# Optimization experiments

Measured on AMD Instinct MI355X. Metric: run time of the kernel, lower is better.

Reference implementation:

```python
import jax, jax.numpy as jnp
import numpy as np

N = 100000   # nodes
E = 1600000  # directed edges (before self loops)
IN = 64
HID = 32     # per-head hidden channels
H = 4        # heads
OUT = 32     # final output channels
NEG_SLOPE = 0.2
LN_EPS = 1e-5


def setup_inputs() -> dict:
    key = jax.random.key(0)
    ks = jax.random.split(key, 24)
    def nrm(k, shape, s=0.1):
        return jax.random.normal(k, shape, jnp.float32) * s
    inp = {
        "x": jax.random.normal(ks[0], (N, IN), jnp.float32),
        "edge_index": jax.random.randint(ks[1], (2, E), 0, N, jnp.int32),
    }
    in_dims = [IN, H * HID, H * HID]
    j = 2
    for i, di in enumerate(in_dims):
        inp[f"W{i}"] = nrm(ks[j], (di, H * HID)); j += 1
        inp[f"as{i}"] = nrm(ks[j], (H, HID)); j += 1
        inp[f"ad{i}"] = nrm(ks[j], (H, HID)); j += 1
        inp[f"b{i}"] = jnp.zeros((H * HID,), jnp.float32)
        inp[f"g{i}"] = jnp.ones((H * HID,), jnp.float32)
        inp[f"be{i}"] = jnp.zeros((H * HID,), jnp.float32)
    inp["Wf"] = nrm(ks[j], (H * HID, OUT)); j += 1
    inp["asf"] = nrm(ks[j], (1, OUT)); j += 1
    inp["adf"] = nrm(ks[j], (1, OUT)); j += 1
    inp["bf"] = jnp.zeros((OUT,), jnp.float32)
    return inp


def gat_conv(x, src, dst, W, att_s, att_d, bias, heads, C, concat, n_nodes):
    # h: [N, H, C]
    h = (x @ W).reshape(n_nodes, heads, C)
    a_src = jnp.sum(h * att_s, axis=-1)  # [N, H]
    a_dst = jnp.sum(h * att_d, axis=-1)  # [N, H]
    e = jax.nn.leaky_relu(a_src[src] + a_dst[dst], NEG_SLOPE)  # [E', H]
    # segment softmax over incoming edges of each dst node
    m = jax.ops.segment_max(e, dst, num_segments=n_nodes)
    m = jnp.where(jnp.isfinite(m), m, 0.0)
    ex = jnp.exp(e - m[dst])
    denom = jax.ops.segment_sum(ex, dst, num_segments=n_nodes)
    alpha = ex / (denom[dst] + 1e-16)  # [E', H]
    msg = h[src] * alpha[..., None]    # [E', H, C]
    out = jax.ops.segment_sum(msg, dst, num_segments=n_nodes)  # [N, H, C]
    if concat:
        out = out.reshape(n_nodes, heads * C)
    else:
        out = out.mean(axis=1)
    return out + bias


def layer_norm(x, g, b):
    mu = x.mean(-1, keepdims=True)
    v = jnp.mean((x - mu) ** 2, axis=-1, keepdims=True)
    return g * (x - mu) / jnp.sqrt(v + LN_EPS) + b


def reference(x, edge_index,
              W0, as0, ad0, b0, g0, be0,
              W1, as1, ad1, b1, g1, be1,
              W2, as2, ad2, b2, g2, be2,
              Wf, asf, adf, bf):
    n_nodes = x.shape[0]
    loop = jnp.arange(n_nodes, dtype=edge_index.dtype)
    src = jnp.concatenate([edge_index[0], loop])  # add self loops (PyG default)
    dst = jnp.concatenate([edge_index[1], loop])
    blocks = [(W0, as0, ad0, b0, g0, be0),
              (W1, as1, ad1, b1, g1, be1),
              (W2, as2, ad2, b2, g2, be2)]
    for (W, a_s, a_d, b, g, be) in blocks:
        x = gat_conv(x, src, dst, W, a_s, a_d, b, H, HID, True, n_nodes)
        x = jax.nn.elu(layer_norm(x, g, be))
    return gat_conv(x, src, dst, Wf, asf, adf, bf, 1, OUT, False, n_nodes)
```

## Files before the change

### kernel.cpp

```cpp
#include <hip/hip_runtime.h>
#include <hip/hip_bf16.h>

constexpr int NN   = 100000;
constexpr int EE   = 1600000;
constexpr int ETOT = EE + NN;
constexpr float SLOPE = 0.2f;
constexpr int BSH = 10;
constexpr int NB  = (NN + (1 << BSH) - 1) >> BSH;
constexpr int CCH = 8192;

typedef __attribute__((ext_vector_type(8))) short short8;
typedef __attribute__((ext_vector_type(4))) float f32x4;

__device__ __forceinline__ float bf_lo(unsigned u) { return __uint_as_float(u << 16); }
__device__ __forceinline__ float bf_hi(unsigned u) { return __uint_as_float(u & 0xffff0000u); }
__device__ __forceinline__ unsigned short f2bf(float f) {
    __hip_bfloat16 h = __float2bfloat16(f);
    return *(unsigned short*)&h;
}
__device__ __forceinline__ void wave_lds_fence() {
    __asm__ volatile("s_waitcnt lgkmcnt(0)" ::: "memory");
}

__global__ void k_cvt_x(const float* __restrict__ x, unsigned short* __restrict__ xb) {
    int i = blockIdx.x * blockDim.x + threadIdx.x;
    if (i >= NN * 64 / 8) return;
    const float4* xp = (const float4*)(x + (size_t)i * 8);
    float4 v0 = xp[0], v1 = xp[1];
    unsigned short o[8] = {f2bf(v0.x), f2bf(v0.y), f2bf(v0.z), f2bf(v0.w),
                           f2bf(v1.x), f2bf(v1.y), f2bf(v1.z), f2bf(v1.w)};
    *(uint4*)(xb + (size_t)i * 8) = *(uint4*)o;
}

__global__ void k_cvt_wt(const float* __restrict__ W, unsigned short* __restrict__ Wt,
                         int K, int N) {
    int i = blockIdx.x * blockDim.x + threadIdx.x;
    if (i >= K * N) return;
    int k = i / N, n = i % N;
    Wt[(size_t)n * K + k] = f2bf(W[i]);
}

__global__ void k_zero(int* p, int n) {
    int i = blockIdx.x * blockDim.x + threadIdx.x;
    if (i < n) p[i] = 0;
}

__global__ __launch_bounds__(256) void k_bhist(const int* __restrict__ ei,
                                               int* __restrict__ gbh) {
    __shared__ int h[NB];
    int t = threadIdx.x;
    if (t < NB) h[t] = 0;
    __syncthreads();
    int i = blockIdx.x * 2048 + t;
#pragma unroll
    for (int k = 0; k < 8; k++, i += 256)
        if (i < EE) atomicAdd(&h[ei[EE + i] >> BSH], 1);
    __syncthreads();
    if (t < NB && h[t]) atomicAdd(&gbh[t], h[t]);
}

__global__ void k_bscan(const int* __restrict__ gbh, int* __restrict__ ebase,
                        int* __restrict__ gcur) {
    __shared__ int sd[128];
    int t = threadIdx.x;
    int v = (t < NB) ? gbh[t] : 0;
    sd[t] = v;
    __syncthreads();
    for (int off = 1; off < 128; off <<= 1) {
        int x = (t >= off) ? sd[t - off] : 0;
        __syncthreads();
        sd[t] += x;
        __syncthreads();
    }
    int ex = sd[t] - v;
    if (t < NB) { ebase[t] = ex; gcur[t] = ex; }
    if (t == NB) ebase[NB] = EE;
}

__global__ __launch_bounds__(256) void k_bscatter(const int* __restrict__ ei,
                                                  int* __restrict__ gcur,
                                                  int* __restrict__ pbuf) {
    __shared__ int h[NB], base[NB], cur[NB];
    int t = threadIdx.x;
    if (t < NB) { h[t] = 0; cur[t] = 0; }
    __syncthreads();
    int c0 = blockIdx.x * CCH;
    int cend = c0 + CCH < EE ? c0 + CCH : EE;
    for (int i = c0 + t; i < cend; i += 256)
        atomicAdd(&h[ei[EE + i] >> BSH], 1);
    __syncthreads();
    if (t < NB && h[t] > 0) base[t] = atomicAdd(&gcur[t], h[t]);
    __syncthreads();
    for (int i = c0 + t; i < cend; i += 256) {
        int s = ei[i], d = ei[EE + i];
        int b = d >> BSH;
        int c = atomicAdd(&cur[b], 1);
        pbuf[base[b] + c] = s | ((d & ((1 << BSH) - 1)) << 17);
    }
}

__global__ __launch_bounds__(256) void k_bcsr(const int* __restrict__ pbuf,
                                              const int* __restrict__ ebase,
                                              int* __restrict__ row_ptr,
                                              int* __restrict__ esrc) {
    constexpr int BNODES = 1 << BSH;
    __shared__ int hist[BNODES];
    __shared__ int cur[BNODES];
    __shared__ int sd[256];
    int b = blockIdx.x, t = threadIdx.x;
    int node0 = b << BSH;
    int e0 = ebase[b], e1 = ebase[b + 1];
    for (int i = t; i < BNODES; i += 256) { hist[i] = 0; cur[i] = 0; }
    __syncthreads();
    for (int i = e0 + t; i < e1; i += 256)
        atomicAdd(&hist[pbuf[i] >> 17], 1);
    __syncthreads();
    int s0 = hist[4 * t], s1 = hist[4 * t + 1], s2 = hist[4 * t + 2], s3 = hist[4 * t + 3];
    int ts = s0 + s1 + s2 + s3;
    sd[t] = ts;
    __syncthreads();
    for (int off = 1; off < 256; off <<= 1) {
        int x = (t >= off) ? sd[t - off] : 0;
        __syncthreads();
        sd[t] += x;
        __syncthreads();
    }
    int ex = sd[t] - ts;
    hist[4 * t] = ex;
    hist[4 * t + 1] = ex + s0;
    hist[4 * t + 2] = ex + s0 + s1;
    hist[4 * t + 3] = ex + s0 + s1 + s2;
    __syncthreads();
    int rbase = e0 + node0;
    for (int nl = t; nl < BNODES; nl += 256) {
        int n = node0 + nl;
        if (n < NN) {
            int rp = rbase + hist[nl] + nl;
            row_ptr[n] = rp;
            esrc[rp] = n;
        }
    }
    __syncthreads();
    for (int i = e0 + t; i < e1; i += 256) {
        int p = pbuf[i];
        int nl = p >> 17;
        int c = atomicAdd(&cur[nl], 1);
        esrc[rbase + hist[nl] + nl + 1 + c] = p & 0x1FFFF;
    }
}

template <int BN, int H>
__global__ __launch_bounds__(256) void k_mfma_att(
    const unsigned short* __restrict__ Ab, const unsigned short* __restrict__ Bt,
    const float* __restrict__ as_, const float* __restrict__ ad_,
    unsigned short* __restrict__ hb, float* __restrict__ a_s,
    float* __restrict__ a_d, int M, int K) {
    constexpr int NCT = BN / 16;
    constexpr int LDK = 72;
    __shared__ unsigned short As[128 * LDK];
    __shared__ unsigned short Bs[BN * LDK];
    int tid = threadIdx.x;
    int lane = tid & 63, w = tid >> 6;
    int q = lane >> 4, col = lane & 15;
    int rowBase = blockIdx.x * 128;

    f32x4 acc[2][NCT];
#pragma unroll
    for (int rt = 0; rt < 2; rt++)
#pragma unroll
        for (int ct = 0; ct < NCT; ct++) acc[rt][ct] = (f32x4){0.f, 0.f, 0.f, 0.f};

    int u = tid & 7;
    int r0 = tid >> 3;
    int nph = K >> 6;
    for (int ph = 0; ph < nph; ph++) {
        int kof = ph * 64 + u * 8;
#pragma unroll
        for (int rr = r0; rr < 128; rr += 32) {
            int gr = rowBase + rr;
            uint4 v = make_uint4(0, 0, 0, 0);
            if (gr < M) v = *(const uint4*)(Ab + (size_t)gr * K + kof);
            *(uint4*)(&As[rr * LDK + u * 8]) = v;
        }
#pragma unroll
        for (int br = r0; br < BN; br += 32) {
            uint4 v = *(const uint4*)(Bt + (size_t)br * K + kof);
            *(uint4*)(&Bs[br * LDK + u * 8]) = v;
        }
        __syncthreads();

        short8 af[2][2];
#pragma unroll
        for (int rt = 0; rt < 2; rt++)
#pragma unroll
            for (int kt = 0; kt < 2; kt++)
                af[rt][kt] = *(const short8*)(&As[(w * 32 + rt * 16 + col) * LDK + kt * 32 + q * 8]);
#pragma unroll
        for (int kt = 0; kt < 2; kt++)
#pragma unroll
            for (int ct = 0; ct < NCT; ct++) {
                short8 bf = *(const short8*)(&Bs[(ct * 16 + col) * LDK + kt * 32 + q * 8]);
#pragma unroll
                for (int rt = 0; rt < 2; rt++)
                    acc[rt][ct] = __builtin_amdgcn_mfma_f32_16x16x32_bf16(
                        af[rt][kt], bf, acc[rt][ct], 0, 0, 0);
            }
        __syncthreads();
    }

    float swv[NCT], dwv[NCT];
#pragma unroll
    for (int ct = 0; ct < NCT; ct++) {
        int c = ct * 16 + col;
        swv[ct] = as_[c];
        dwv[ct] = ad_[c];
    }
#pragma unroll
    for (int rt = 0; rt < 2; rt++) {
#pragma unroll
        for (int r = 0; r < 4; r++) {
            int gr = rowBase + w * 32 + rt * 16 + q * 4 + r;
            if constexpr (H == 4) {
                float ps[4] = {0, 0, 0, 0}, pd[4] = {0, 0, 0, 0};
#pragma unroll
                for (int ct = 0; ct < NCT; ct++) {
                    float v = acc[rt][ct][r];
                    ps[ct >> 1] += v * swv[ct];
                    pd[ct >> 1] += v * dwv[ct];
                }
#pragma unroll
                for (int m = 1; m < 16; m <<= 1)
#pragma unroll
                    for (int h = 0; h < 4; h++) {
                        ps[h] += __shfl_xor(ps[h], m);
                        pd[h] += __shfl_xor(pd[h], m);
                    }
                if (gr < M) {
#pragma unroll
                    for (int ct = 0; ct < NCT; ct++)
                        hb[(size_t)gr * BN + ct * 16 + col] = f2bf(acc[rt][ct][r]);
                    if (col == 0) {
                        *(float4*)(a_s + (size_t)gr * 4) = make_float4(ps[0], ps[1], ps[2], ps[3]);
                        *(float4*)(a_d + (size_t)gr * 4) = make_float4(pd[0], pd[1], pd[2], pd[3]);
                    }
                }
            } else {
                float ps = 0.f, pd = 0.f;
#pragma unroll
                for (int ct = 0; ct < NCT; ct++) {
                    float v = acc[rt][ct][r];
                    ps += v * swv[ct];
                    pd += v * dwv[ct];
                }
#pragma unroll
                for (int m = 1; m < 16; m <<= 1) {
                    ps += __shfl_xor(ps, m);
                    pd += __shfl_xor(pd, m);
                }
                if (gr < M) {
#pragma unroll
                    for (int ct = 0; ct < NCT; ct++)
                        hb[(size_t)gr * BN + ct * 16 + col] = f2bf(acc[rt][ct][r]);
                    if (col == 0) { a_s[gr] = ps; a_d[gr] = pd; }
                }
            }
        }
    }
}

__global__ __launch_bounds__(256) void k_aggregate_ln(
    const unsigned short* __restrict__ hb, const float* __restrict__ a_src,
    const float* __restrict__ a_dst, const int* __restrict__ row_ptr,
    const int* __restrict__ esrc, const float* __restrict__ bias,
    const float* __restrict__ gamma, const float* __restrict__ beta,
    unsigned short* __restrict__ xb) {
    __shared__ uint2 slab_all[4][64 * 5];
    int lane = threadIdx.x & 63;
    int w = threadIdx.x >> 6;
    uint2* slab = slab_all[w];
    int n = blockIdx.x * 4 + w;
    if (n >= NN) return;
    int start = row_ptr[n];
    int end = (n == NN - 1) ? ETOT : row_ptr[n + 1];
    int deg = end - start;

    float4 ad = ((const float4*)a_dst)[n];
    int g = lane >> 4, c16 = lane & 15, head = c16 >> 2;
    float acc[8];
#pragma unroll
    for (int k = 0; k < 8; k++) acc[k] = 0.f;

    if (deg <= 64) {
        int msrc = 0;
        float me0 = 0.f, me1 = 0.f, me2 = 0.f, me3 = 0.f;
        if (lane < deg) {
            int s = esrc[start + lane];
            msrc = s;
            float4 a = ((const float4*)a_src)[s];
            float e0 = a.x + ad.x; e0 = e0 > 0.f ? e0 : SLOPE * e0; me0 = __expf(e0);
            float e1 = a.y + ad.y; e1 = e1 > 0.f ? e1 : SLOPE * e1; me1 = __expf(e1);
            float e2 = a.z + ad.z; e2 = e2 > 0.f ? e2 : SLOPE * e2; me2 = __expf(e2);
            float e3 = a.w + ad.w; e3 = e3 > 0.f ? e3 : SLOPE * e3; me3 = __expf(e3);
        }
        float d0 = me0, d1 = me1, d2 = me2, d3 = me3;
#pragma unroll
        for (int m = 1; m < 64; m <<= 1) {
            d0 += __shfl_xor(d0, m);
            d1 += __shfl_xor(d1, m);
            d2 += __shfl_xor(d2, m);
            d3 += __shfl_xor(d3, m);
        }
        me0 *= 1.f / (d0 + 1e-16f);
        me1 *= 1.f / (d1 + 1e-16f);
        me2 *= 1.f / (d2 + 1e-16f);
        me3 *= 1.f / (d3 + 1e-16f);
        if (lane < deg) {
            slab[lane * 5 + 0] = make_uint2((unsigned)msrc, __float_as_uint(me0));
            slab[lane * 5 + 1] = make_uint2((unsigned)msrc, __float_as_uint(me1));
            slab[lane * 5 + 2] = make_uint2((unsigned)msrc, __float_as_uint(me2));
            slab[lane * 5 + 3] = make_uint2((unsigned)msrc, __float_as_uint(me3));
        }
        wave_lds_fence();
        int iters = (deg + 3) >> 2;
        for (int it = 0; it < iters; it++) {
            int j = g + (it << 2);
            if (j < deg) {
                uint2 p = slab[j * 5 + head];
                int s = (int)p.x;
                float al = __uint_as_float(p.y);
                uint4 uu = *(const uint4*)(hb + (size_t)s * 128 + c16 * 8);
                acc[0] += bf_lo(uu.x) * al; acc[1] += bf_hi(uu.x) * al;
                acc[2] += bf_lo(uu.y) * al; acc[3] += bf_hi(uu.y) * al;
                acc[4] += bf_lo(uu.z) * al; acc[5] += bf_hi(uu.z) * al;
                acc[6] += bf_lo(uu.w) * al; acc[7] += bf_hi(uu.w) * al;
            }
        }
    } else {
        float d0 = 0.f, d1 = 0.f, d2 = 0.f, d3 = 0.f;
        for (int k = start + lane; k < end; k += 64) {
            int s = esrc[k];
            float4 a = ((const float4*)a_src)[s];
            float e0 = a.x + ad.x; e0 = e0 > 0.f ? e0 : SLOPE * e0; d0 += __expf(e0);
            float e1 = a.y + ad.y; e1 = e1 > 0.f ? e1 : SLOPE * e1; d1 += __expf(e1);
            float e2 = a.z + ad.z; e2 = e2 > 0.f ? e2 : SLOPE * e2; d2 += __expf(e2);
            float e3 = a.w + ad.w; e3 = e3 > 0.f ? e3 : SLOPE * e3; d3 += __expf(e3);
        }
#pragma unroll
        for (int m = 1; m < 64; m <<= 1) {
            d0 += __shfl_xor(d0, m);
            d1 += __shfl_xor(d1, m);
            d2 += __shfl_xor(d2, m);
            d3 += __shfl_xor(d3, m);
        }
        float invh = head == 0 ? 1.f / (d0 + 1e-16f) : head == 1 ? 1.f / (d1 + 1e-16f)
                   : head == 2 ? 1.f / (d2 + 1e-16f) : 1.f / (d3 + 1e-16f);
        float adh = head == 0 ? ad.x : head == 1 ? ad.y : head == 2 ? ad.z : ad.w;
        for (int j = g; j < deg; j += 4) {
            int s = esrc[start + j];
            float e = a_src[(size_t)s * 4 + head] + adh;
            e = e > 0.f ? e : SLOPE * e;
            float al = __expf(e) * invh;
            uint4 uu = *(const uint4*)(hb + (size_t)s * 128 + c16 * 8);
            acc[0] += bf_lo(uu.x) * al; acc[1] += bf_hi(uu.x) * al;
            acc[2] += bf_lo(uu.y) * al; acc[3] += bf_hi(uu.y) * al;
            acc[4] += bf_lo(uu.z) * al; acc[5] += bf_hi(uu.z) * al;
            acc[6] += bf_lo(uu.w) * al; acc[7] += bf_hi(uu.w) * al;
        }
    }

#pragma unroll
    for (int k = 0; k < 8; k++) {
        acc[k] += __shfl_xor(acc[k], 16);
        acc[k] += __shfl_xor(acc[k], 32);
    }
    if (lane < 16) {
        float y[8];
        float sum = 0.f;
        const float4* bp = (const float4*)(bias + lane * 8);
        float4 b0 = bp[0], b1 = bp[1];
#pragma unroll
        for (int k = 0; k < 8; k++) {
            float b = k < 4 ? (&b0.x)[k] : (&b1.x)[k - 4];
            y[k] = acc[k] + b;
            sum += y[k];
        }
#pragma unroll
        for (int m = 1; m < 16; m <<= 1) sum += __shfl_xor(sum, m);
        float mu = sum * (1.f / 128.f);
        float ss = 0.f;
        float d[8];
#pragma unroll
        for (int k = 0; k < 8; k++) { d[k] = y[k] - mu; ss += d[k] * d[k]; }
#pragma unroll
        for (int m = 1; m < 16; m <<= 1) ss += __shfl_xor(ss, m);
        float is = rsqrtf(ss * (1.f / 128.f) + 1e-5f);
        const float4* gp = (const float4*)(gamma + lane * 8);
        const float4* ep = (const float4*)(beta + lane * 8);
        float4 g0 = gp[0], g1 = gp[1], e0 = ep[0], e1 = ep[1];
        unsigned short o16[8];
#pragma unroll
        for (int k = 0; k < 8; k++) {
            float gm = k < 4 ? (&g0.x)[k] : (&g1.x)[k - 4];
            float bt = k < 4 ? (&e0.x)[k] : (&e1.x)[k - 4];
            float z = gm * (d[k] * is) + bt;
            o16[k] = f2bf(z > 0.f ? z : __expf(z) - 1.f);
        }
        *(uint4*)(xb + (size_t)n * 128 + lane * 8) = *(uint4*)o16;
    }
}

__global__ __launch_bounds__(256) void k_agg_final(
    const unsigned short* __restrict__ hb, const float* __restrict__ a_src,
    const float* __restrict__ a_dst, const int* __restrict__ row_ptr,
    const int* __restrict__ esrc, const float* __restrict__ bf,
    float* __restrict__ out) {
    __shared__ uint2 slab_all[4][64];
    int lane = threadIdx.x & 63;
    int w = threadIdx.x >> 6;
    uint2* slab = slab_all[w];
    int n = blockIdx.x * 4 + w;
    if (n >= NN) return;
    int start = row_ptr[n];
    int end = (n == NN - 1) ? ETOT : row_ptr[n + 1];
    int deg = end - start;
    float adn = a_dst[n];

    int g = lane >> 3, c8 = lane & 7;
    float acc[4] = {0.f, 0.f, 0.f, 0.f};

    if (deg <= 64) {
        int msrc = 0;
        float me = 0.f;
        if (lane < deg) {
            int s = esrc[start + lane];
            msrc = s;
            float e = a_src[s] + adn;
            e = e > 0.f ? e : SLOPE * e;
            me = __expf(e);
        }
        float d = me;
#pragma unroll
        for (int m = 1; m < 64; m <<= 1) d += __shfl_xor(d, m);
        me *= 1.f / (d + 1e-16f);
        if (lane < deg) slab[lane] = make_uint2((unsigned)msrc, __float_as_uint(me));
        wave_lds_fence();
        int iters = (deg + 7) >> 3;
        for (int it = 0; it < iters; it++) {
            int j = g + (it << 3);
            if (j < deg) {
                uint2 p = slab[j];
                int s = (int)p.x;
                float al = __uint_as_float(p.y);
                uint2 u = *(const uint2*)(hb + (size_t)s * 32 + c8 * 4);
                acc[0] += bf_lo(u.x) * al; acc[1] += bf_hi(u.x) * al;
                acc[2] += bf_lo(u.y) * al; acc[3] += bf_hi(u.y) * al;
            }
        }
    } else {
        float d = 0.f;
        for (int k = start + lane; k < end; k += 64) {
            int s = esrc[k];
            float e = a_src[s] + adn;
            e = e > 0.f ? e : SLOPE * e;
            d += __expf(e);
        }
#pragma unroll
        for (int m = 1; m < 64; m <<= 1) d += __shfl_xor(d, m);
        float inv = 1.f / (d + 1e-16f);
        for (int j = g; j < deg; j += 8) {
            int s = esrc[start + j];
            float e = a_src[s] + adn;
            e = e > 0.f ? e : SLOPE * e;
            float al = __expf(e) * inv;
            uint2 u = *(const uint2*)(hb + (size_t)s * 32 + c8 * 4);
            acc[0] += bf_lo(u.x) * al; acc[1] += bf_hi(u.x) * al;
            acc[2] += bf_lo(u.y) * al; acc[3] += bf_hi(u.y) * al;
        }
    }
#pragma unroll
    for (int k = 0; k < 4; k++) {
        acc[k] += __shfl_xor(acc[k], 8);
        acc[k] += __shfl_xor(acc[k], 16);
        acc[k] += __shfl_xor(acc[k], 32);
    }
    if (lane < 8) {
        float4 b4 = ((const float4*)bf)[lane];
        float4 o = make_float4(acc[0] + b4.x, acc[1] + b4.y, acc[2] + b4.z,
                               acc[3] + b4.w);
        ((float4*)out)[(size_t)n * 8 + lane] = o;
    }
}

extern "C" void kernel_launch(void* const* d_in, const int* in_sizes, int n_in,
                              void* d_out, int out_size, void* d_ws,
                              size_t ws_size, hipStream_t stream) {
    const float* x  = (const float*)d_in[0];
    const int* ei   = (const int*)d_in[1];
    const float* W[3]  = {(const float*)d_in[2], (const float*)d_in[8],  (const float*)d_in[14]};
    const float* AS[3] = {(const float*)d_in[3], (const float*)d_in[9],  (const float*)d_in[15]};
    const float* AD[3] = {(const float*)d_in[4], (const float*)d_in[10], (const float*)d_in[16]};
    const float* Bb[3] = {(const float*)d_in[5], (const float*)d_in[11], (const float*)d_in[17]};
    const float* G[3]  = {(const float*)d_in[6], (const float*)d_in[12], (const float*)d_in[18]};
    const float* BE[3] = {(const float*)d_in[7], (const float*)d_in[13], (const float*)d_in[19]};
    const float* Wf  = (const float*)d_in[20];
    const float* asf = (const float*)d_in[21];
    const float* adf = (const float*)d_in[22];
    const float* bfp = (const float*)d_in[23];
    float* out = (float*)d_out;

    unsigned short* xb = (unsigned short*)d_ws;
    unsigned short* hb = xb + (size_t)NN * 128;
    float* a_s = (float*)(hb + (size_t)NN * 128);
    float* a_d = a_s + (size_t)NN * 4;
    int* row_ptr = (int*)(a_d + (size_t)NN * 4);
    int* esrc    = row_ptr + NN;
    int* gbh     = esrc + ETOT;
    int* ebase   = gbh + NB;
    int* gcur    = ebase + NB + 1;
    int* pbuf    = gcur + NB;
    unsigned short* Wt0 = (unsigned short*)(pbuf + EE);
    unsigned short* Wt1 = Wt0 + 128 * 64;
    unsigned short* Wt2 = Wt1 + 128 * 128;
    unsigned short* Wtf = Wt2 + 128 * 128;

    k_cvt_x<<<(NN * 64 / 8 + 255) / 256, 256, 0, stream>>>(x, xb);
    k_cvt_wt<<<(64 * 128 + 255) / 256, 256, 0, stream>>>(W[0], Wt0, 64, 128);
    k_cvt_wt<<<(128 * 128 + 255) / 256, 256, 0, stream>>>(W[1], Wt1, 128, 128);
    k_cvt_wt<<<(128 * 128 + 255) / 256, 256, 0, stream>>>(W[2], Wt2, 128, 128);
    k_cvt_wt<<<(128 * 32 + 255) / 256, 256, 0, stream>>>(Wf, Wtf, 128, 32);

    k_zero<<<1, 128, 0, stream>>>(gbh, NB);
    k_bhist<<<(EE + 2047) / 2048, 256, 0, stream>>>(ei, gbh);
    k_bscan<<<1, 128, 0, stream>>>(gbh, ebase, gcur);
    k_bscatter<<<(EE + CCH - 1) / CCH, 256, 0, stream>>>(ei, gcur, pbuf);
    k_bcsr<<<NB, 256, 0, stream>>>(pbuf, ebase, row_ptr, esrc);

    const unsigned short* Wts[3] = {Wt0, Wt1, Wt2};
    int K = 64;
    int gblk = (NN + 127) / 128;
    for (int l = 0; l < 3; l++) {
        k_mfma_att<128, 4><<<gblk, 256, 0, stream>>>(xb, Wts[l], AS[l], AD[l],
                                                     hb, a_s, a_d, NN, K);
        k_aggregate_ln<<<(NN + 3) / 4, 256, 0, stream>>>(hb, a_s, a_d, row_ptr,
                                                         esrc, Bb[l], G[l], BE[l], xb);
        K = 128;
    }
    k_mfma_att<32, 1><<<gblk, 256, 0, stream>>>(xb, Wtf, asf, adf, hb, a_s, a_d,
                                                NN, 128);
    k_agg_final<<<(NN + 3) / 4, 256, 0, stream>>>(hb, a_s, a_d, row_ptr, esrc,
                                                  bfp, out);
}
```

Measured before the change: 596.6 us.

## Aggregate four nodes per wave with 16-lane groups in GAT aggregate+LN kernel

Restructures the hidden-layer aggregation kernel so each 64-lane wave handles four destination nodes, one per 16-lane group, instead of one node per wave. Per-edge exp weights and sources are staged in per-node LDS slabs, and each group walks its node's edges serially with full 16-lane feature loads. This removes the idle lanes the old layout had for average degree around 17. Waves whose max degree exceeds a cap fall back to a per-node loop that uses shuffles instead of LDS. It also replaces the leaky-relu select with fmaxf.

```diff
diff --git a/kernel.cpp b/kernel.cpp
--- a/kernel.cpp
+++ b/kernel.cpp
@@ -8,6 +8,7 @@
 constexpr int BSH = 10;
 constexpr int NB  = (NN + (1 << BSH) - 1) >> BSH;
 constexpr int CCH = 8192;
+constexpr int DCAP = 48;
 
 typedef __attribute__((ext_vector_type(8))) short short8;
 typedef __attribute__((ext_vector_type(4))) float f32x4;
@@ -274,138 +275,225 @@
     const int* __restrict__ esrc, const float* __restrict__ bias,
     const float* __restrict__ gamma, const float* __restrict__ beta,
     unsigned short* __restrict__ xb) {
-    __shared__ uint2 slab_all[4][64 * 5];
-    int lane = threadIdx.x & 63;
-    int w = threadIdx.x >> 6;
+    __shared__ uint2 slab_all[4][4 * 4 * DCAP];
+    int tid = threadIdx.x;
+    int w = tid >> 6, lane = tid & 63;
+    int g = lane >> 4, i = lane & 15;
+    int myhead = i >> 2;
     uint2* slab = slab_all[w];
-    int n = blockIdx.x * 4 + w;
-    if (n >= NN) return;
-    int start = row_ptr[n];
-    int end = (n == NN - 1) ? ETOT : row_ptr[n + 1];
-    int deg = end - start;
-
-    float4 ad = ((const float4*)a_dst)[n];
-    int g = lane >> 4, c16 = lane & 15, head = c16 >> 2;
-    float acc[8];
-#pragma unroll
-    for (int k = 0; k < 8; k++) acc[k] = 0.f;
-
-    if (deg <= 64) {
-        int msrc = 0;
-        float me0 = 0.f, me1 = 0.f, me2 = 0.f, me3 = 0.f;
-        if (lane < deg) {
-            int s = esrc[start + lane];
-            msrc = s;
+    int n0 = blockIdx.x * 16 + w * 4;
+    int n = n0 + g;
+    bool valid = n < NN;
+    int start = 0, deg = 0;
+    if (valid) {
+        start = row_ptr[n];
+        int end = (n == NN - 1) ? ETOT : row_ptr[n + 1];
+        deg = end - start;
+    }
+    int wmax = deg;
+#pragma unroll
+    for (int m = 1; m < 64; m <<= 1) wmax = max(wmax, __shfl_xor(wmax, m));
+
+    if (wmax <= DCAP) {
+        float4 ad = make_float4(0.f, 0.f, 0.f, 0.f);
+        if (valid) ad = ((const float4*)a_dst)[n];
+        float d0 = 0.f, d1 = 0.f, d2 = 0.f, d3 = 0.f;
+        uint2* nslab = slab + g * (4 * DCAP);
+        for (int k = i; k < deg; k += 16) {
+            int s = esrc[start + k];
             float4 a = ((const float4*)a_src)[s];
-            float e0 = a.x + ad.x; e0 = e0 > 0.f ? e0 : SLOPE * e0; me0 = __expf(e0);
-            float e1 = a.y + ad.y; e1 = e1 > 0.f ? e1 : SLOPE * e1; me1 = __expf(e1);
-            float e2 = a.z + ad.z; e2 = e2 > 0.f ? e2 : SLOPE * e2; me2 = __expf(e2);
-            float e3 = a.w + ad.w; e3 = e3 > 0.f ? e3 : SLOPE * e3; me3 = __expf(e3);
-        }
-        float d0 = me0, d1 = me1, d2 = me2, d3 = me3;
-#pragma unroll
-        for (int m = 1; m < 64; m <<= 1) {
+            float e0 = a.x + ad.x; e0 = fmaxf(e0, SLOPE * e0); float x0 = __expf(e0);
+            float e1 = a.y + ad.y; e1 = fmaxf(e1, SLOPE * e1); float x1 = __expf(e1);
+            float e2 = a.z + ad.z; e2 = fmaxf(e2, SLOPE * e2); float x2 = __expf(e2);
+            float e3 = a.w + ad.w; e3 = fmaxf(e3, SLOPE * e3); float x3 = __expf(e3);
+            nslab[0 * DCAP + k] = make_uint2((unsigned)s, __float_as_uint(x0));
+            nslab[1 * DCAP + k] = make_uint2((unsigned)s, __float_as_uint(x1));
+            nslab[2 * DCAP + k] = make_uint2((unsigned)s, __float_as_uint(x2));
+            nslab[3 * DCAP + k] = make_uint2((unsigned)s, __float_as_uint(x3));
+            d0 += x0; d1 += x1; d2 += x2; d3 += x3;
+        }
+#pragma unroll
+        for (int m = 1; m < 16; m <<= 1) {
             d0 += __shfl_xor(d0, m);
             d1 += __shfl_xor(d1, m);
             d2 += __shfl_xor(d2, m);
             d3 += __shfl_xor(d3, m);
         }
-        me0 *= 1.f / (d0 + 1e-16f);
-        me1 *= 1.f / (d1 + 1e-16f);
-        me2 *= 1.f / (d2 + 1e-16f);
-        me3 *= 1.f / (d3 + 1e-16f);
-        if (lane < deg) {
-            slab[lane * 5 + 0] = make_uint2((unsigned)msrc, __float_as_uint(me0));
-            slab[lane * 5 + 1] = make_uint2((unsigned)msrc, __float_as_uint(me1));
-            slab[lane * 5 + 2] = make_uint2((unsigned)msrc, __float_as_uint(me2));
-            slab[lane * 5 + 3] = make_uint2((unsigned)msrc, __float_as_uint(me3));
-        }
+        float dh = myhead == 0 ? d0 : myhead == 1 ? d1 : myhead == 2 ? d2 : d3;
+        float inv = 1.f / (dh + 1e-16f);
         wave_lds_fence();
-        int iters = (deg + 3) >> 2;
-        for (int it = 0; it < iters; it++) {
-            int j = g + (it << 2);
-            if (j < deg) {
-                uint2 p = slab[j * 5 + head];
-                int s = (int)p.x;
-                float al = __uint_as_float(p.y);
-                uint4 uu = *(const uint4*)(hb + (size_t)s * 128 + c16 * 8);
-                acc[0] += bf_lo(uu.x) * al; acc[1] += bf_hi(uu.x) * al;
-                acc[2] += bf_lo(uu.y) * al; acc[3] += bf_hi(uu.y) * al;
-                acc[4] += bf_lo(uu.z) * al; acc[5] += bf_hi(uu.z) * al;
-                acc[6] += bf_lo(uu.w) * al; acc[7] += bf_hi(uu.w) * al;
-            }
-        }
-    } else {
-        float d0 = 0.f, d1 = 0.f, d2 = 0.f, d3 = 0.f;
-        for (int k = start + lane; k < end; k += 64) {
-            int s = esrc[k];
-            float4 a = ((const float4*)a_src)[s];
-            float e0 = a.x + ad.x; e0 = e0 > 0.f ? e0 : SLOPE * e0; d0 += __expf(e0);
-            float e1 = a.y + ad.y; e1 = e1 > 0.f ? e1 : SLOPE * e1; d1 += __expf(e1);
-            float e2 = a.z + ad.z; e2 = e2 > 0.f ? e2 : SLOPE * e2; d2 += __expf(e2);
-            float e3 = a.w + ad.w; e3 = e3 > 0.f ? e3 : SLOPE * e3; d3 += __expf(e3);
-        }
-#pragma unroll
-        for (int m = 1; m < 64; m <<= 1) {
-            d0 += __shfl_xor(d0, m);
-            d1 += __shfl_xor(d1, m);
-            d2 += __shfl_xor(d2, m);
-            d3 += __shfl_xor(d3, m);
-        }
-        float invh = head == 0 ? 1.f / (d0 + 1e-16f) : head == 1 ? 1.f / (d1 + 1e-16f)
-                   : head == 2 ? 1.f / (d2 + 1e-16f) : 1.f / (d3 + 1e-16f);
-        float adh = head == 0 ? ad.x : head == 1 ? ad.y : head == 2 ? ad.z : ad.w;
-        for (int j = g; j < deg; j += 4) {
-            int s = esrc[start + j];
-            float e = a_src[(size_t)s * 4 + head] + adh;
-            e = e > 0.f ? e : SLOPE * e;
-            float al = __expf(e) * invh;
-            uint4 uu = *(const uint4*)(hb + (size_t)s * 128 + c16 * 8);
+
+        float acc[8];
+#pragma unroll
+        for (int k = 0; k < 8; k++) acc[k] = 0.f;
+        const uint2* myrow = nslab + myhead * DCAP;
+        for (int j = 0; j < deg; j++) {
+            uint2 p = myrow[j];
+            float al = __uint_as_float(p.y) * inv;
+            uint4 uu = *(const uint4*)(hb + (size_t)p.x * 128 + i * 8);
             acc[0] += bf_lo(uu.x) * al; acc[1] += bf_hi(uu.x) * al;
             acc[2] += bf_lo(uu.y) * al; acc[3] += bf_hi(uu.y) * al;
             acc[4] += bf_lo(uu.z) * al; acc[5] += bf_hi(uu.z) * al;
             acc[6] += bf_lo(uu.w) * al; acc[7] += bf_hi(uu.w) * al;
         }
-    }
-
-#pragma unroll
-    for (int k = 0; k < 8; k++) {
-        acc[k] += __shfl_xor(acc[k], 16);
-        acc[k] += __shfl_xor(acc[k], 32);
-    }
-    if (lane < 16) {
-        float y[8];
-        float sum = 0.f;
-        const float4* bp = (const float4*)(bias + lane * 8);
-        float4 b0 = bp[0], b1 = bp[1];
-#pragma unroll
-        for (int k = 0; k < 8; k++) {
-            float b = k < 4 ? (&b0.x)[k] : (&b1.x)[k - 4];
-            y[k] = acc[k] + b;
-            sum += y[k];
-        }
-#pragma unroll
-        for (int m = 1; m < 16; m <<= 1) sum += __shfl_xor(sum, m);
-        float mu = sum * (1.f / 128.f);
-        float ss = 0.f;
-        float d[8];
-#pragma unroll
-        for (int k = 0; k < 8; k++) { d[k] = y[k] - mu; ss += d[k] * d[k]; }
-#pragma unroll
-        for (int m = 1; m < 16; m <<= 1) ss += __shfl_xor(ss, m);
-        float is = rsqrtf(ss * (1.f / 128.f) + 1e-5f);
-        const float4* gp = (const float4*)(gamma + lane * 8);
-        const float4* ep = (const float4*)(beta + lane * 8);
-        float4 g0 = gp[0], g1 = gp[1], e0 = ep[0], e1 = ep[1];
-        unsigned short o16[8];
-#pragma unroll
-        for (int k = 0; k < 8; k++) {
-            float gm = k < 4 ? (&g0.x)[k] : (&g1.x)[k - 4];
-            float bt = k < 4 ? (&e0.x)[k] : (&e1.x)[k - 4];
-            float z = gm * (d[k] * is) + bt;
-            o16[k] = f2bf(z > 0.f ? z : __expf(z) - 1.f);
-        }
-        *(uint4*)(xb + (size_t)n * 128 + lane * 8) = *(uint4*)o16;
+        if (valid) {
+            float y[8];
+            float sum = 0.f;
+            const float4* bp = (const float4*)(bias + i * 8);
+            float4 b0 = bp[0], b1 = bp[1];
+#pragma unroll
+            for (int k = 0; k < 8; k++) {
+                float b = k < 4 ? (&b0.x)[k] : (&b1.x)[k - 4];
+                y[k] = acc[k] + b;
+                sum += y[k];
+            }
+#pragma unroll
+            for (int m = 1; m < 16; m <<= 1) sum += __shfl_xor(sum, m);
+            float mu = sum * (1.f / 128.f);
+            float ss = 0.f;
+            float d[8];
+#pragma unroll
+            for (int k = 0; k < 8; k++) { d[k] = y[k] - mu; ss += d[k] * d[k]; }
+#pragma unroll
+            for (int m = 1; m < 16; m <<= 1) ss += __shfl_xor(ss, m);
+            float is = rsqrtf(ss * (1.f / 128.f) + 1e-5f);
+            const float4* gp = (const float4*)(gamma + i * 8);
+            const float4* ep = (const float4*)(beta + i * 8);
+            float4 g0 = gp[0], g1 = gp[1], e0 = ep[0], e1 = ep[1];
+            unsigned short o16[8];
+#pragma unroll
+            for (int k = 0; k < 8; k++) {
+                float gm = k < 4 ? (&g0.x)[k] : (&g1.x)[k - 4];
+                float bt = k < 4 ? (&e0.x)[k] : (&e1.x)[k - 4];
+                float z = gm * (d[k] * is) + bt;
+                o16[k] = f2bf(z > 0.f ? z : __expf(z) - 1.f);
+            }
+            *(uint4*)(xb + (size_t)n * 128 + i * 8) = *(uint4*)o16;
+        }
+    } else {
+        for (int m4 = 0; m4 < 4; m4++) {
+            int nm = n0 + m4;
+            if (nm >= NN) continue;
+            int startm = row_ptr[nm];
+            int endm = (nm == NN - 1) ? ETOT : row_ptr[nm + 1];
+            int degm = endm - startm;
+            float4 ad = ((const float4*)a_dst)[nm];
+            int gg = lane >> 4, c16 = lane & 15, hh = c16 >> 2;
+            float acc[8];
+#pragma unroll
+            for (int k = 0; k < 8; k++) acc[k] = 0.f;
+            if (degm <= 64) {
+                int msrc = 0;
+                float me0 = 0.f, me1 = 0.f, me2 = 0.f, me3 = 0.f;
+                if (lane < degm) {
+                    int s = esrc[startm + lane];
+                    msrc = s;
+                    float4 a = ((const float4*)a_src)[s];
+                    float e0 = a.x + ad.x; e0 = fmaxf(e0, SLOPE * e0); me0 = __expf(e0);
+                    float e1 = a.y + ad.y; e1 = fmaxf(e1, SLOPE * e1); me1 = __expf(e1);
+                    float e2 = a.z + ad.z; e2 = fmaxf(e2, SLOPE * e2); me2 = __expf(e2);
+                    float e3 = a.w + ad.w; e3 = fmaxf(e3, SLOPE * e3); me3 = __expf(e3);
+                }
+                float d0 = me0, d1 = me1, d2 = me2, d3 = me3;
+#pragma unroll
+                for (int m = 1; m < 64; m <<= 1) {
+                    d0 += __shfl_xor(d0, m);
+                    d1 += __shfl_xor(d1, m);
+                    d2 += __shfl_xor(d2, m);
+                    d3 += __shfl_xor(d3, m);
+                }
+                me0 *= 1.f / (d0 + 1e-16f);
+                me1 *= 1.f / (d1 + 1e-16f);
+                me2 *= 1.f / (d2 + 1e-16f);
+                me3 *= 1.f / (d3 + 1e-16f);
+                int iters = (degm + 3) >> 2;
+                for (int it = 0; it < iters; it++) {
+                    int j = gg + (it << 2);
+                    int jj = j < degm ? j : 0;
+                    int s = __shfl(msrc, jj);
+                    float a0 = __shfl(me0, jj), a1 = __shfl(me1, jj);
+                    float a2 = __shfl(me2, jj), a3 = __shfl(me3, jj);
+                    if (j < degm) {
+                        float al = hh == 0 ? a0 : hh == 1 ? a1 : hh == 2 ? a2 : a3;
+                        uint4 uu = *(const uint4*)(hb + (size_t)s * 128 + c16 * 8);
+                        acc[0] += bf_lo(uu.x) * al; acc[1] += bf_hi(uu.x) * al;
+                        acc[2] += bf_lo(uu.y) * al; acc[3] += bf_hi(uu.y) * al;
+                        acc[4] += bf_lo(uu.z) * al; acc[5] += bf_hi(uu.z) * al;
+                        acc[6] += bf_lo(uu.w) * al; acc[7] += bf_hi(uu.w) * al;
+                    }
+                }
+            } else {
+                float d0 = 0.f, d1 = 0.f, d2 = 0.f, d3 = 0.f;
+                for (int k = startm + lane; k < endm; k += 64) {
+                    int s = esrc[k];
+                    float4 a = ((const float4*)a_src)[s];
+                    float e0 = a.x + ad.x; e0 = fmaxf(e0, SLOPE * e0); d0 += __expf(e0);
+                    float e1 = a.y + ad.y; e1 = fmaxf(e1, SLOPE * e1); d1 += __expf(e1);
+                    float e2 = a.z + ad.z; e2 = fmaxf(e2, SLOPE * e2); d2 += __expf(e2);
+                    float e3 = a.w + ad.w; e3 = fmaxf(e3, SLOPE * e3); d3 += __expf(e3);
+                }
+#pragma unroll
+                for (int m = 1; m < 64; m <<= 1) {
+                    d0 += __shfl_xor(d0, m);
+                    d1 += __shfl_xor(d1, m);
+                    d2 += __shfl_xor(d2, m);
+                    d3 += __shfl_xor(d3, m);
+                }
+                float invh = hh == 0 ? 1.f / (d0 + 1e-16f) : hh == 1 ? 1.f / (d1 + 1e-16f)
+                           : hh == 2 ? 1.f / (d2 + 1e-16f) : 1.f / (d3 + 1e-16f);
+                float adh = hh == 0 ? ad.x : hh == 1 ? ad.y : hh == 2 ? ad.z : ad.w;
+                for (int j = gg; j < degm; j += 4) {
+                    int s = esrc[startm + j];
+                    float e = a_src[(size_t)s * 4 + hh] + adh;
+                    e = fmaxf(e, SLOPE * e);
+                    float al = __expf(e) * invh;
+                    uint4 uu = *(const uint4*)(hb + (size_t)s * 128 + c16 * 8);
+                    acc[0] += bf_lo(uu.x) * al; acc[1] += bf_hi(uu.x) * al;
+                    acc[2] += bf_lo(uu.y) * al; acc[3] += bf_hi(uu.y) * al;
+                    acc[4] += bf_lo(uu.z) * al; acc[5] += bf_hi(uu.z) * al;
+                    acc[6] += bf_lo(uu.w) * al; acc[7] += bf_hi(uu.w) * al;
+                }
+            }
+#pragma unroll
+            for (int k = 0; k < 8; k++) {
+                acc[k] += __shfl_xor(acc[k], 16);
+                acc[k] += __shfl_xor(acc[k], 32);
+            }
+            if (lane < 16) {
+                float y[8];
+                float sum = 0.f;
+                const float4* bp = (const float4*)(bias + lane * 8);
+                float4 b0 = bp[0], b1 = bp[1];
+#pragma unroll
+                for (int k = 0; k < 8; k++) {
+                    float b = k < 4 ? (&b0.x)[k] : (&b1.x)[k - 4];
+                    y[k] = acc[k] + b;
+                    sum += y[k];
+                }
+#pragma unroll
+                for (int m = 1; m < 16; m <<= 1) sum += __shfl_xor(sum, m);
+                float mu = sum * (1.f / 128.f);
+                float ss = 0.f;
+                float d[8];
+#pragma unroll
+                for (int k = 0; k < 8; k++) { d[k] = y[k] - mu; ss += d[k] * d[k]; }
+#pragma unroll
+                for (int m = 1; m < 16; m <<= 1) ss += __shfl_xor(ss, m);
+                float is = rsqrtf(ss * (1.f / 128.f) + 1e-5f);
+                const float4* gp = (const float4*)(gamma + lane * 8);
+                const float4* ep = (const float4*)(beta + lane * 8);
+                float4 g0 = gp[0], g1 = gp[1], e0 = ep[0], e1 = ep[1];
+                unsigned short o16[8];
+#pragma unroll
+                for (int k = 0; k < 8; k++) {
+                    float gm = k < 4 ? (&g0.x)[k] : (&g1.x)[k - 4];
+                    float bt = k < 4 ? (&e0.x)[k] : (&e1.x)[k - 4];
+                    float z = gm * (d[k] * is) + bt;
+                    o16[k] = f2bf(z > 0.f ? z : __expf(z) - 1.f);
+                }
+                *(uint4*)(xb + (size_t)nm * 128 + lane * 8) = *(uint4*)o16;
+            }
+        }
     }
 }
 
@@ -435,7 +523,7 @@
             int s = esrc[start + lane];
             msrc = s;
             float e = a_src[s] + adn;
-            e = e > 0.f ? e : SLOPE * e;
+            e = fmaxf(e, SLOPE * e);
             me = __expf(e);
         }
         float d = me;
@@ -461,7 +549,7 @@
         for (int k = start + lane; k < end; k += 64) {
             int s = esrc[k];
             float e = a_src[s] + adn;
-            e = e > 0.f ? e : SLOPE * e;
+            e = fmaxf(e, SLOPE * e);
             d += __expf(e);
         }
 #pragma unroll
@@ -470,7 +558,7 @@
         for (int j = g; j < deg; j += 8) {
             int s = esrc[start + j];
             float e = a_src[s] + adn;
-            e = e > 0.f ? e : SLOPE * e;
+            e = fmaxf(e, SLOPE * e);
             float al = __expf(e) * inv;
             uint2 u = *(const uint2*)(hb + (size_t)s * 32 + c8 * 4);
             acc[0] += bf_lo(u.x) * al; acc[1] += bf_hi(u.x) * al;
@@ -541,8 +629,8 @@
     for (int l = 0; l < 3; l++) {
         k_mfma_att<128, 4><<<gblk, 256, 0, stream>>>(xb, Wts[l], AS[l], AD[l],
                                                      hb, a_s, a_d, NN, K);
-        k_aggregate_ln<<<(NN + 3) / 4, 256, 0, stream>>>(hb, a_s, a_d, row_ptr,
-                                                         esrc, Bb[l], G[l], BE[l], xb);
+        k_aggregate_ln<<<(NN + 15) / 16, 256, 0, stream>>>(hb, a_s, a_d, row_ptr,
+                                                           esrc, Bb[l], G[l], BE[l], xb);
         K = 128;
     }
     k_mfma_att<32, 1><<<gblk, 256, 0, stream>>>(xb, Wtf, asf, adf, hb, a_s, a_d,
```

Result: faster. 560.6 us (-6.0%).
